# Performance work log

Measured on AMD Instinct MI355X. Metric: run time of the kernel, lower is better.

Reference implementation:

```python
import jax, jax.numpy as jnp
import numpy as np

D = 512
FV = 50000
EV = 50000
SRC = 128
TGT = 129  # BOS + 128 targets


def setup_inputs() -> dict:
    key = jax.random.key(0)
    ks = jax.random.split(key, 16)
    s = 0.02  # init scale
    return {
        "fnums": jax.random.randint(ks[0], (SRC,), 0, FV, dtype=jnp.int32),
        "enums": jax.random.randint(ks[1], (TGT,), 0, EV, dtype=jnp.int32),
        "emb_f": jax.random.normal(ks[2], (FV, D), jnp.float32) * s,
        "Wih_e": jax.random.normal(ks[3], (D, D), jnp.float32) * s,
        "Whh_e": jax.random.normal(ks[4], (D, D), jnp.float32) * s,
        "b_e": jnp.zeros((D,), jnp.float32),
        "h0_e": jax.random.normal(ks[5], (D,), jnp.float32) * s,
        "emb_d": jax.random.normal(ks[6], (EV, D), jnp.float32) * s,
        "Wih_d": jax.random.normal(ks[7], (D, D), jnp.float32) * s,
        "Whh_d": jax.random.normal(ks[8], (D, D), jnp.float32) * s,
        "b_d": jnp.zeros((D,), jnp.float32),
        "h0_d": jax.random.normal(ks[9], (D,), jnp.float32) * s,
        "Wm": jax.random.normal(ks[10], (D, 2 * D), jnp.float32) * s,
        "bm": jnp.zeros((D,), jnp.float32),
        "Wo": jax.random.normal(ks[11], (EV, D), jnp.float32) * s,
        "bo": jnp.zeros((EV,), jnp.float32),
    }


def reference(fnums, enums, emb_f, Wih_e, Whh_e, b_e, h0_e,
              emb_d, Wih_d, Whh_d, b_d, h0_d, Wm, bm, Wo, bo):
    # --- Encoder: vanilla tanh RNN over source embeddings ---
    xs = emb_f[fnums]  # (SRC, D)

    def enc_step(h, x):
        h2 = jnp.tanh(x @ Wih_e.T + h @ Whh_e.T + b_e)
        return h2, h2

    _, fencs = jax.lax.scan(enc_step, h0_e, xs)  # (SRC, D)

    # --- Decoder: teacher-forced log-probability of enums[1:] given enums[:-1] ---
    inp = enums[:-1]
    tgt = enums[1:]

    def dec_step(h, it):
        i, t = it
        e = emb_d[i]                                   # (D,)
        h2 = jnp.tanh(e @ Wih_d.T + h @ Whh_d.T + b_d)  # new RNN state o == h2
        scores = fencs @ h2                             # (SRC,) dot-product attention
        alpha = jax.nn.softmax(scores)
        c = alpha @ fencs                               # (D,) context
        m = jnp.tanh(jnp.concatenate([c, h2]) @ Wm.T + bm)
        lp = jax.nn.log_softmax(m @ Wo.T + bo)          # (EV,)
        return h2, lp[t]

    _, lps = jax.lax.scan(dec_step, h0_d, (inp, tgt))
    return jnp.sum(lps)  # scalar log-probability of the sentence pair
```

## Files before the change

### kernel.cpp

```cpp
#include <hip/hip_runtime.h>
#include <stdint.h>

#define D      512
#define NSTEP  128
#define EVOC   50000
#define VTILE  128
#define NBV    ((EVOC + VTILE - 1) / VTILE)
#define LDA_W  36
#define LDB_W  132
#define WM16   (D / 16)
#define WO16   ((EVOC + 15) / 16)

typedef unsigned int u32x4 __attribute__((ext_vector_type(4)));

__device__ inline int sdot4(int a, int b, int c) {
#if __has_builtin(__builtin_amdgcn_sdot4)
    return __builtin_amdgcn_sdot4(a, b, c, false);
#else
    int r = c;
    r += (int)(int8_t)(a)       * (int)(int8_t)(b);
    r += (int)(int8_t)(a >> 8)  * (int)(int8_t)(b >> 8);
    r += (int)(int8_t)(a >> 16) * (int)(int8_t)(b >> 16);
    r += (int)(int8_t)(a >> 24) * (int)(int8_t)(b >> 24);
    return r;
#endif
}

__device__ inline int sdot8(uint32_t a, uint32_t b, int c) {
#if __has_builtin(__builtin_amdgcn_sdot8)
    return __builtin_amdgcn_sdot8((int)a, (int)b, c, false);
#else
    int r = c;
    #pragma unroll
    for (int k = 0; k < 8; k++) {
        int av = ((int)(a << (28 - 4 * k))) >> 28;
        int bv = ((int)(b << (28 - 4 * k))) >> 28;
        r += av * bv;
    }
    return r;
#endif
}

__device__ inline int rdlane(uint32_t v, int k) {
#if __has_builtin(__builtin_amdgcn_readlane)
    return (int)__builtin_amdgcn_readlane(v, k);
#else
    return (int)__shfl((int)v, k, 64);
#endif
}

__device__ inline uint32_t pack4(float a, float b, float c, float d, float inv) {
    return  ((uint32_t)(uint8_t)(int8_t)__float2int_rn(a * inv)) |
            ((uint32_t)(uint8_t)(int8_t)__float2int_rn(b * inv) << 8) |
            ((uint32_t)(uint8_t)(int8_t)__float2int_rn(c * inv) << 16) |
            ((uint32_t)(uint8_t)(int8_t)__float2int_rn(d * inv) << 24);
}

__device__ inline float amax4(float4 v) {
    return fmaxf(fmaxf(fabsf(v.x), fabsf(v.y)), fmaxf(fabsf(v.z), fabsf(v.w)));
}

__global__ __launch_bounds__(256) void k_prep2(
        const float* __restrict__ We,   const float* __restrict__ Wd,
        const int* __restrict__ fnums,  const int* __restrict__ enums,
        const float* __restrict__ emb_f,const float* __restrict__ emb_d,
        const float* __restrict__ Wih_e,const float* __restrict__ Wih_d,
        const float* __restrict__ b_e,  const float* __restrict__ b_d,
        uint32_t* __restrict__ q4, float* __restrict__ qsc,
        float* __restrict__ pre_e, float* __restrict__ pre_d) {
    __shared__ float xl[D];
    int bid = blockIdx.x, t = threadIdx.x;
    if (bid < 256) {
        int rg = bid * 4 + (t >> 6);
        int which = rg >> 9, row = rg & 511;
        int lane = t & 63;
        const float* W = which ? Wd : We;
        const float* src = W + (size_t)row * D + lane * 8;
        float w[8];
        #pragma unroll
        for (int k = 0; k < 8; k++) w[k] = src[k];
        float m = 0.f;
        #pragma unroll
        for (int k = 0; k < 8; k++) m = fmaxf(m, fabsf(w[k]));
        for (int off = 32; off; off >>= 1) m = fmaxf(m, __shfl_xor(m, off));
        float inv = (m > 0.f) ? 7.f / m : 0.f;
        uint32_t word = 0;
        #pragma unroll
        for (int k = 0; k < 8; k++) {
            int q = max(-7, min(7, __float2int_rn(w[k] * inv)));
            word |= ((uint32_t)(q & 0xF)) << (4 * k);
        }
        int hf = lane >> 5, c = (lane & 31) >> 2, wi = lane & 3;
        q4[((size_t)which * 8192 + (size_t)c * 1024 + (hf << 9) + row) * 4 + wi] = word;
        if (lane == 0) qsc[which * D + row] = m / 7.f;
    } else {
        int bb = bid - 256;
        int kind = bb >> 7, s = bb & 127;
        const float* emb = kind ? emb_d : emb_f;
        int idx          = kind ? enums[s] : fnums[s];
        const float* W   = kind ? Wih_d : Wih_e;
        const float* b   = kind ? b_d : b_e;
        float* pre       = kind ? pre_d : pre_e;
        xl[t]       = emb[(size_t)idx * D + t];
        xl[t + 256] = emb[(size_t)idx * D + t + 256];
        __syncthreads();
        for (int rep = 0; rep < 2; rep++) {
            int o = t + rep * 256;
            float acc = b[o];
            const float4* Wr = (const float4*)(W + (size_t)o * D);
            #pragma unroll 8
            for (int k4 = 0; k4 < D / 4; k4++) {
                float4 w = Wr[k4];
                acc += w.x * xl[4*k4] + w.y * xl[4*k4+1] + w.z * xl[4*k4+2] + w.w * xl[4*k4+3];
            }
            pre[(size_t)s * D + o] = acc;
        }
    }
}

__global__ __launch_bounds__(1024)
__attribute__((amdgpu_waves_per_eu(4, 4)))
void k_scan_fused(
        const uint32_t* __restrict__ q4, const float* __restrict__ qsc,
        const float* __restrict__ pre_e, const float* __restrict__ pre_d,
        const float* __restrict__ h0_e, const float* __restrict__ h0_d,
        float* __restrict__ fencs, float* __restrict__ h2s,
        const float* __restrict__ Wm, const float* __restrict__ Wo,
        int8_t* __restrict__ wmq, float* __restrict__ wmsc,
        uint32_t* __restrict__ woq2, float* __restrict__ wosc) {
    __shared__ __align__(16) uint32_t wlds[16384];
    __shared__ __align__(4) uint32_t hq4[2][64];
    __shared__ int pacc[D];
    int bid = blockIdx.x, t = threadIdx.x;

    if (bid >= 2) {
        int lane = t & 63, sub = t >> 6;
        if (bid < 2 + WM16) {
            int row = (bid - 2) * 16 + sub;
            const float4* src = (const float4*)(Wm + (size_t)row * 2 * D);
            float4 a = src[lane], b = src[lane + 64], c = src[lane + 128], d2 = src[lane + 192];
            float m = fmaxf(fmaxf(amax4(a), amax4(b)), fmaxf(amax4(c), amax4(d2)));
            for (int off = 32; off; off >>= 1) m = fmaxf(m, __shfl_xor(m, off));
            float inv = (m > 0.f) ? 127.f / m : 0.f;
            uint32_t* dst = (uint32_t*)(wmq + (size_t)row * 2 * D);
            dst[lane]       = pack4(a.x, a.y, a.z, a.w, inv);
            dst[lane + 64]  = pack4(b.x, b.y, b.z, b.w, inv);
            dst[lane + 128] = pack4(c.x, c.y, c.z, c.w, inv);
            dst[lane + 192] = pack4(d2.x, d2.y, d2.z, d2.w, inv);
            if (lane == 0) wmsc[row] = m / 127.f;
        } else {
            int row = (bid - 2 - WM16) * 16 + sub;
            if (row < EVOC) {
                const float4* src = (const float4*)(Wo + (size_t)row * D);
                float4 v0 = src[lane], v1 = src[lane + 64];
                float m = fmaxf(amax4(v0), amax4(v1));
                for (int off = 32; off; off >>= 1) m = fmaxf(m, __shfl_xor(m, off));
                float inv = (m > 0.f) ? 127.f / m : 0.f;
                uint32_t w1 = pack4(v0.x, v0.y, v0.z, v0.w, inv);
                uint32_t w2 = pack4(v1.x, v1.y, v1.z, v1.w, inv);
                int wA = lane, wB = lane + 64;
                woq2[((size_t)(row >> 7) * 4 + (wA >> 5)) * 4096 + (size_t)(row & 127) * 32 + (wA & 31)] = w1;
                woq2[((size_t)(row >> 7) * 4 + (wB >> 5)) * 4096 + (size_t)(row & 127) * 32 + (wB & 31)] = w2;
                if (lane == 0) wosc[row] = m / 127.f;
            }
        }
        return;
    }

    int lane = t & 63;
    int hf = t >> 9;
    int r  = t & 511;
    int which = bid;
    const float* pre = which ? pre_d : pre_e;
    const float* h0  = which ? h0_d : h0_e;
    float*       hs  = which ? h2s : fencs;
    float sw = qsc[which * D + r] * (1.f / 7.f);
    const u32x4* wq = (const u32x4*)q4 + (size_t)which * 8192 + t;

    u32x4* wl = (u32x4*)wlds;
    #pragma unroll
    for (int c = 0; c < 4; c++) wl[c * 1024 + t] = wq[c * 1024];

    if (hf == 0) {
        float h0v = fminf(fmaxf(h0[r], -0.999f), 0.999f);
        int nib = max(-7, min(7, __float2int_rn(h0v * 7.f)));
        uint32_t mynib = (uint32_t)(nib & 0xF);
        uint32_t other = (uint32_t)__shfl_xor((int)mynib, 1);
        if (!(r & 1))
            ((uint8_t*)&hq4[0][0])[r >> 1] = (uint8_t)(mynib | (other << 4));
    }
    __syncthreads();

    int p = 0;
    for (int step = 0; step < NSTEP; step++) {
        uint32_t own = hq4[p][(hf << 5) | (lane & 31)];
        u32x4 g0 = wq[4 * 1024], g1 = wq[5 * 1024], g2 = wq[6 * 1024], g3 = wq[7 * 1024];
        u32x4 l0 = wl[t], l1 = wl[1024 + t], l2 = wl[2048 + t], l3 = wl[3072 + t];
        int a0 = 0, a1 = 0;
        #define DOTC(c, wv) {                                          \
            a0 = sdot8((wv).x, (uint32_t)rdlane(own, (c) * 4 + 0), a0);\
            a1 = sdot8((wv).y, (uint32_t)rdlane(own, (c) * 4 + 1), a1);\
            a0 = sdot8((wv).z, (uint32_t)rdlane(own, (c) * 4 + 2), a0);\
            a1 = sdot8((wv).w, (uint32_t)rdlane(own, (c) * 4 + 3), a1); }
        DOTC(0, l0) DOTC(1, l1) DOTC(2, l2) DOTC(3, l3)
        DOTC(4, g0) DOTC(5, g1) DOTC(6, g2) DOTC(7, g3)
        #undef DOTC
        int acc = a0 + a1;
        if (hf) pacc[r] = acc;
        __syncthreads();
        if (!hf) {
            int tot = acc + pacc[r];
            float h2 = tanhf(pre[(size_t)step * D + r] + (float)tot * sw);
            hs[(size_t)step * D + r] = h2;
            int nib = max(-7, min(7, __float2int_rn(h2 * 7.f)));
            uint32_t mynib = (uint32_t)(nib & 0xF);
            uint32_t other = (uint32_t)__shfl_xor((int)mynib, 1);
            if (!(r & 1))
                ((uint8_t*)&hq4[p ^ 1][0])[r >> 1] = (uint8_t)(mynib | (other << 4));
        }
        __syncthreads();
        p ^= 1;
    }
}

__global__ __launch_bounds__(512) void k_att1(
        const float* __restrict__ fencs, const float* __restrict__ h2s,
        int8_t* __restrict__ chq) {
    __shared__ float h2l[D], sc[NSTEP], red[64];
    __shared__ float ftile[32 * D];
    int s = blockIdx.x, t = threadIdx.x;
    h2l[t] = h2s[(size_t)s * D + t];
    __syncthreads();

    {
        int j = t >> 2, q = t & 3;
        const float4* fr = (const float4*)(fencs + (size_t)j * D + q * 128);
        const float4* hr = (const float4*)(h2l + q * 128);
        float acc = 0.f;
        #pragma unroll 8
        for (int k4 = 0; k4 < 32; k4++) {
            float4 f = fr[k4], hh = hr[k4];
            acc += f.x*hh.x + f.y*hh.y + f.z*hh.z + f.w*hh.w;
        }
        acc += __shfl_xor(acc, 1);
        acc += __shfl_xor(acc, 2);
        if (q == 0) sc[j] = acc;
    }
    __syncthreads();
    if (t < 64) {
        float m = fmaxf(sc[t], sc[t + 64]);
        for (int off = 32; off; off >>= 1) m = fmaxf(m, __shfl_xor(m, off));
        if (t == 0) red[0] = m;
    }
    __syncthreads();
    float mx = red[0];
    __syncthreads();
    if (t < NSTEP) sc[t] = expf(sc[t] - mx);
    __syncthreads();
    if (t < 64) {
        float v = sc[t] + sc[t + 64];
        for (int off = 32; off; off >>= 1) v += __shfl_xor(v, off);
        if (t == 0) red[0] = v;
    }
    __syncthreads();
    float inv = 1.0f / red[0];

    float cacc = 0.f;
    for (int jt = 0; jt < 4; jt++) {
        #pragma unroll
        for (int k = 0; k < 32; k++)
            ftile[t + k * D] = fencs[(size_t)jt * 32 * D + t + k * D];
        __syncthreads();
        #pragma unroll 8
        for (int j = 0; j < 32; j++)
            cacc += sc[jt * 32 + j] * ftile[j * D + t];
        __syncthreads();
    }
    float cv = cacc * inv;
    chq[(size_t)s * 2 * D + t]     = (int8_t)__float2int_rn(cv * 127.f);
    chq[(size_t)s * 2 * D + D + t] = (int8_t)__float2int_rn(h2l[t] * 127.f);
}

__global__ __launch_bounds__(512) void k_att2(
        const int8_t* __restrict__ chq, const int8_t* __restrict__ wmq,
        const float* __restrict__ wmsc, const float* __restrict__ bm,
        int8_t* __restrict__ mq) {
    __shared__ __align__(16) uint32_t a_s[128 * LDA_W];
    __shared__ __align__(16) uint32_t b_s[32 * LDB_W];
    int t = threadIdx.x;
    int v0 = blockIdx.x * VTILE;
    int ti = t >> 5, tj = t & 31;
    int lrow = t >> 3, lq = t & 7;
    int acc[8][4] = {};

    for (int kc = 0; kc < 8; kc++) {
        #pragma unroll
        for (int rep = 0; rep < 2; rep++) {
            int row = lrow + rep * 64;
            uint4 av = *(const uint4*)(chq + (size_t)row * 2 * D + kc * 128 + lq * 16);
            *(uint4*)&a_s[row * LDA_W + lq * 4] = av;
            int v = v0 + row;
            uint4 bv = *(const uint4*)(wmq + (size_t)v * 2 * D + kc * 128 + lq * 16);
            b_s[(lq*4+0) * LDB_W + row] = bv.x;
            b_s[(lq*4+1) * LDB_W + row] = bv.y;
            b_s[(lq*4+2) * LDB_W + row] = bv.z;
            b_s[(lq*4+3) * LDB_W + row] = bv.w;
        }
        __syncthreads();
        #pragma unroll
        for (int q = 0; q < 8; q++) {
            uint4 aw[8];
            #pragma unroll
            for (int i = 0; i < 8; i++)
                aw[i] = *(const uint4*)&a_s[(ti*8 + i) * LDA_W + q*4];
            #pragma unroll
            for (int k4 = 0; k4 < 4; k4++) {
                uint4 bw = *(const uint4*)&b_s[(q*4 + k4) * LDB_W + tj * 4];
                #pragma unroll
                for (int i = 0; i < 8; i++) {
                    uint32_t a = (k4 == 0) ? aw[i].x : (k4 == 1) ? aw[i].y
                               : (k4 == 2) ? aw[i].z : aw[i].w;
                    acc[i][0] = sdot4((int)a, (int)bw.x, acc[i][0]);
                    acc[i][1] = sdot4((int)a, (int)bw.y, acc[i][1]);
                    acc[i][2] = sdot4((int)a, (int)bw.z, acc[i][2]);
                    acc[i][3] = sdot4((int)a, (int)bw.w, acc[i][3]);
                }
            }
        }
        __syncthreads();
    }

    float sw4[4], bm4[4];
    #pragma unroll
    for (int jj = 0; jj < 4; jj++) {
        int col = v0 + tj * 4 + jj;
        sw4[jj] = wmsc[col] * (1.f / (127.f * 127.f));
        bm4[jj] = bm[col];
    }
    #pragma unroll
    for (int i = 0; i < 8; i++) {
        int s = ti * 8 + i;
        float m0 = tanhf((float)acc[i][0] * sw4[0] + bm4[0]);
        float m1 = tanhf((float)acc[i][1] * sw4[1] + bm4[1]);
        float m2 = tanhf((float)acc[i][2] * sw4[2] + bm4[2]);
        float m3 = tanhf((float)acc[i][3] * sw4[3] + bm4[3]);
        ((uint32_t*)mq)[(size_t)s * (D / 4) + (v0 >> 2) + tj] = pack4(m0, m1, m2, m3, 127.f);
    }
}

__global__ __launch_bounds__(512) void k_logits(
        const int8_t* __restrict__ mq, const uint32_t* __restrict__ woq2,
        const float* __restrict__ wosc, const float* __restrict__ bo,
        const int* __restrict__ enums,
        float* __restrict__ pmax, float* __restrict__ psum, float* __restrict__ pick) {
    __shared__ __align__(16) uint32_t a_s[128 * LDA_W];
    __shared__ __align__(16) uint32_t b_s[32 * LDB_W];
    int b = blockIdx.x, t = threadIdx.x;
    int v0 = b * VTILE;
    int ti = t >> 5, tj = t & 31;
    int lrow = t >> 3, lq = t & 7;
    int acc[8][4] = {};

    for (int kc = 0; kc < 4; kc++) {
        const uint4* bsrc = (const uint4*)(woq2 + ((size_t)b * 4 + kc) * 4096);
        #pragma unroll
        for (int rep = 0; rep < 2; rep++) {
            int row = lrow + rep * 64;
            uint4 av = *(const uint4*)(mq + (size_t)row * D + kc * 128 + lq * 16);
            *(uint4*)&a_s[row * LDA_W + lq * 4] = av;
            uint4 bv = bsrc[t + rep * 512];
            b_s[(lq*4+0) * LDB_W + row] = bv.x;
            b_s[(lq*4+1) * LDB_W + row] = bv.y;
            b_s[(lq*4+2) * LDB_W + row] = bv.z;
            b_s[(lq*4+3) * LDB_W + row] = bv.w;
        }
        __syncthreads();
        #pragma unroll
        for (int q = 0; q < 8; q++) {
            uint4 aw[8];
            #pragma unroll
            for (int i = 0; i < 8; i++)
                aw[i] = *(const uint4*)&a_s[(ti*8 + i) * LDA_W + q*4];
            #pragma unroll
            for (int k4 = 0; k4 < 4; k4++) {
                uint4 bw = *(const uint4*)&b_s[(q*4 + k4) * LDB_W + tj * 4];
                #pragma unroll
                for (int i = 0; i < 8; i++) {
                    uint32_t a = (k4 == 0) ? aw[i].x : (k4 == 1) ? aw[i].y
                               : (k4 == 2) ? aw[i].z : aw[i].w;
                    acc[i][0] = sdot4((int)a, (int)bw.x, acc[i][0]);
                    acc[i][1] = sdot4((int)a, (int)bw.y, acc[i][1]);
                    acc[i][2] = sdot4((int)a, (int)bw.z, acc[i][2]);
                    acc[i][3] = sdot4((int)a, (int)bw.w, acc[i][3]);
                }
            }
        }
        __syncthreads();
    }

    float sw4[4], bo4[4];
    int vld[4];
    #pragma unroll
    for (int jj = 0; jj < 4; jj++) {
        int v = v0 + tj * 4 + jj;
        vld[jj] = (v < EVOC);
        sw4[jj] = vld[jj] ? wosc[v] * (1.f / 127.f) : 0.f;
        bo4[jj] = vld[jj] ? bo[v] : 0.f;
    }
    #pragma unroll
    for (int i = 0; i < 8; i++) {
        int s = ti * 8 + i;
        float l[4];
        float mx = -1e30f;
        #pragma unroll
        for (int jj = 0; jj < 4; jj++) {
            l[jj] = vld[jj] ? (float)acc[i][jj] * sw4[jj] + bo4[jj] : -1e30f;
            mx = fmaxf(mx, l[jj]);
        }
        #pragma unroll
        for (int off = 1; off < 32; off <<= 1) mx = fmaxf(mx, __shfl_xor(mx, off));
        float sm = 0.f;
        #pragma unroll
        for (int jj = 0; jj < 4; jj++)
            if (vld[jj]) sm += expf(l[jj] - mx);
        #pragma unroll
        for (int off = 1; off < 32; off <<= 1) sm += __shfl_xor(sm, off);
        if (tj == 0) { pmax[b * NSTEP + s] = mx; psum[b * NSTEP + s] = sm; }
        int tgt = enums[s + 1];
        if (tgt >= v0 && tgt < v0 + VTILE) {
            int c = tgt - v0;
            if ((c >> 2) == tj) pick[s] = l[c & 3];
        }
    }
}

__global__ __launch_bounds__(256) void k_final_par(
        const float* __restrict__ pmax, const float* __restrict__ psum,
        const float* __restrict__ pick, float* __restrict__ lp) {
    __shared__ float red[8];
    int s = blockIdx.x, t = threadIdx.x;
    float M = -1e30f;
    for (int b = t; b < NBV; b += 256) M = fmaxf(M, pmax[b * NSTEP + s]);
    for (int off = 32; off; off >>= 1) M = fmaxf(M, __shfl_xor(M, off));
    if ((t & 63) == 0) red[t >> 6] = M;
    __syncthreads();
    M = fmaxf(fmaxf(red[0], red[1]), fmaxf(red[2], red[3]));
    float S = 0.f;
    for (int b = t; b < NBV; b += 256) S += psum[b * NSTEP + s] * expf(pmax[b * NSTEP + s] - M);
    for (int off = 32; off; off >>= 1) S += __shfl_xor(S, off);
    if ((t & 63) == 0) red[4 + (t >> 6)] = S;
    __syncthreads();
    if (t == 0) {
        S = red[4] + red[5] + red[6] + red[7];
        lp[s] = pick[s] - (M + logf(S));
    }
}

__global__ void k_final_sum(const float* __restrict__ lp, float* __restrict__ out) {
    __shared__ float red[NSTEP];
    int t = threadIdx.x;
    red[t] = lp[t];
    __syncthreads();
    for (int off = 64; off > 0; off >>= 1) {
        if (t < off) red[t] += red[t + off];
        __syncthreads();
    }
    if (t == 0) out[0] = red[0];
}

extern "C" void kernel_launch(void* const* d_in, const int* in_sizes, int n_in,
                              void* d_out, int out_size, void* d_ws, size_t ws_size,
                              hipStream_t stream) {
    const int*   fnums = (const int*)  d_in[0];
    const int*   enums = (const int*)  d_in[1];
    const float* emb_f = (const float*)d_in[2];
    const float* Wih_e = (const float*)d_in[3];
    const float* Whh_e = (const float*)d_in[4];
    const float* b_e   = (const float*)d_in[5];
    const float* h0_e  = (const float*)d_in[6];
    const float* emb_d = (const float*)d_in[7];
    const float* Wih_d = (const float*)d_in[8];
    const float* Whh_d = (const float*)d_in[9];
    const float* b_d   = (const float*)d_in[10];
    const float* h0_d  = (const float*)d_in[11];
    const float* Wm    = (const float*)d_in[12];
    const float* bm    = (const float*)d_in[13];
    const float* Wo    = (const float*)d_in[14];
    const float* bo    = (const float*)d_in[15];

    float* ws = (float*)d_ws;
    float* pre_e = ws;
    float* pre_d = ws + 65536;
    float* fencs = ws + 131072;
    float* h2s   = ws + 196608;
    float* pmax  = ws + 262144;
    float* psum  = ws + 312192;
    float* pick  = ws + 362240;
    float* lp    = ws + 362368;
    float* qsc   = ws + 362496;
    float* wmsc  = ws + 363520;
    float* wosc  = ws + 364032;
    uint32_t* q4 = (uint32_t*)(ws + 414080);
    int8_t*   wmq  = (int8_t*)(ws + 479616);
    int8_t*   chq  = (int8_t*)(ws + 610688);
    int8_t*   mq   = (int8_t*)(ws + 643456);
    uint32_t* woq2 = (uint32_t*)(ws + 659840);

    k_prep2<<<dim3(512), dim3(256), 0, stream>>>(
        Whh_e, Whh_d, fnums, enums, emb_f, emb_d, Wih_e, Wih_d, b_e, b_d,
        q4, qsc, pre_e, pre_d);
    k_scan_fused<<<dim3(2 + WM16 + WO16), dim3(1024), 0, stream>>>(
        q4, qsc, pre_e, pre_d, h0_e, h0_d, fencs, h2s,
        Wm, Wo, wmq, wmsc, woq2, wosc);
    k_att1<<<dim3(NSTEP), dim3(512), 0, stream>>>(fencs, h2s, chq);
    k_att2<<<dim3(4), dim3(512), 0, stream>>>(chq, wmq, wmsc, bm, mq);
    k_logits<<<dim3(NBV), dim3(512), 0, stream>>>(mq, woq2, wosc, bo, enums, pmax, psum, pick);
    k_final_par<<<dim3(NSTEP), dim3(256), 0, stream>>>(pmax, psum, pick, lp);
    k_final_sum<<<dim3(1), dim3(NSTEP), 0, stream>>>(lp, (float*)d_out);
}
```

Measured before the change: 273.4 us.

## Use one thread per hidden row in the recurrent scan to drop the cross-half reduction

The recurrent scan kernel drops from 1024 to 512 threads per block, so each thread computes a full 512-wide row dot product instead of half of one. This removes the shared-memory partial-sum exchange and one block barrier per step. Half of the quantized weight row stays in LDS and half is loaded from global memory each step. The int4 weight layout produced by the prep kernel is changed to match, and the side blocks that quantize Wm and Wo now handle 8 rows each, so twice as many blocks are launched. The cost is twice the serial dot-product work per thread and more registers per thread.

```diff
diff --git a/kernel.cpp b/kernel.cpp
--- a/kernel.cpp
+++ b/kernel.cpp
@@ -8,8 +8,8 @@
 #define NBV    ((EVOC + VTILE - 1) / VTILE)
 #define LDA_W  36
 #define LDB_W  132
-#define WM16   (D / 16)
-#define WO16   ((EVOC + 15) / 16)
+#define WM8    (D / 8)
+#define WO8    ((EVOC + 7) / 8)
 
 typedef unsigned int u32x4 __attribute__((ext_vector_type(4)));
 
@@ -90,8 +90,7 @@
             int q = max(-7, min(7, __float2int_rn(w[k] * inv)));
             word |= ((uint32_t)(q & 0xF)) << (4 * k);
         }
-        int hf = lane >> 5, c = (lane & 31) >> 2, wi = lane & 3;
-        q4[((size_t)which * 8192 + (size_t)c * 1024 + (hf << 9) + row) * 4 + wi] = word;
+        q4[((size_t)which * 8192 + (size_t)(lane >> 2) * 512 + row) * 4 + (lane & 3)] = word;
         if (lane == 0) qsc[which * D + row] = m / 7.f;
     } else {
         int bb = bid - 256;
@@ -118,7 +117,7 @@
     }
 }
 
-__global__ __launch_bounds__(1024)
+__global__ __launch_bounds__(512)
 __attribute__((amdgpu_waves_per_eu(4, 4)))
 void k_scan_fused(
         const uint32_t* __restrict__ q4, const float* __restrict__ qsc,
@@ -130,13 +129,12 @@
         uint32_t* __restrict__ woq2, float* __restrict__ wosc) {
     __shared__ __align__(16) uint32_t wlds[16384];
     __shared__ __align__(4) uint32_t hq4[2][64];
-    __shared__ int pacc[D];
     int bid = blockIdx.x, t = threadIdx.x;
 
     if (bid >= 2) {
         int lane = t & 63, sub = t >> 6;
-        if (bid < 2 + WM16) {
-            int row = (bid - 2) * 16 + sub;
+        if (bid < 2 + WM8) {
+            int row = (bid - 2) * 8 + sub;
             const float4* src = (const float4*)(Wm + (size_t)row * 2 * D);
             float4 a = src[lane], b = src[lane + 64], c = src[lane + 128], d2 = src[lane + 192];
             float m = fmaxf(fmaxf(amax4(a), amax4(b)), fmaxf(amax4(c), amax4(d2)));
@@ -149,7 +147,7 @@
             dst[lane + 192] = pack4(d2.x, d2.y, d2.z, d2.w, inv);
             if (lane == 0) wmsc[row] = m / 127.f;
         } else {
-            int row = (bid - 2 - WM16) * 16 + sub;
+            int row = (bid - 2 - WM8) * 8 + sub;
             if (row < EVOC) {
                 const float4* src = (const float4*)(Wo + (size_t)row * D);
                 float4 v0 = src[lane], v1 = src[lane + 64];
@@ -168,8 +166,7 @@
     }
 
     int lane = t & 63;
-    int hf = t >> 9;
-    int r  = t & 511;
+    int r = t;
     int which = bid;
     const float* pre = which ? pre_d : pre_e;
     const float* h0  = which ? h0_d : h0_e;
@@ -179,9 +176,9 @@
 
     u32x4* wl = (u32x4*)wlds;
     #pragma unroll
-    for (int c = 0; c < 4; c++) wl[c * 1024 + t] = wq[c * 1024];
-
-    if (hf == 0) {
+    for (int c = 0; c < 8; c++) wl[c * 512 + t] = wq[c * 512];
+
+    {
         float h0v = fminf(fmaxf(h0[r], -0.999f), 0.999f);
         int nib = max(-7, min(7, __float2int_rn(h0v * 7.f)));
         uint32_t mynib = (uint32_t)(nib & 0xF);
@@ -193,31 +190,34 @@
 
     int p = 0;
     for (int step = 0; step < NSTEP; step++) {
-        uint32_t own = hq4[p][(hf << 5) | (lane & 31)];
-        u32x4 g0 = wq[4 * 1024], g1 = wq[5 * 1024], g2 = wq[6 * 1024], g3 = wq[7 * 1024];
-        u32x4 l0 = wl[t], l1 = wl[1024 + t], l2 = wl[2048 + t], l3 = wl[3072 + t];
-        int a0 = 0, a1 = 0;
-        #define DOTC(c, wv) {                                          \
-            a0 = sdot8((wv).x, (uint32_t)rdlane(own, (c) * 4 + 0), a0);\
-            a1 = sdot8((wv).y, (uint32_t)rdlane(own, (c) * 4 + 1), a1);\
-            a0 = sdot8((wv).z, (uint32_t)rdlane(own, (c) * 4 + 2), a0);\
-            a1 = sdot8((wv).w, (uint32_t)rdlane(own, (c) * 4 + 3), a1); }
-        DOTC(0, l0) DOTC(1, l1) DOTC(2, l2) DOTC(3, l3)
-        DOTC(4, g0) DOTC(5, g1) DOTC(6, g2) DOTC(7, g3)
+        uint32_t own = hq4[p][lane];
+        u32x4 g0 = wq[8 * 512],  g1 = wq[9 * 512],  g2 = wq[10 * 512], g3 = wq[11 * 512];
+        u32x4 g4 = wq[12 * 512], g5 = wq[13 * 512], g6 = wq[14 * 512], g7 = wq[15 * 512];
+        int a0 = 0, a1 = 0, a2 = 0, a3 = 0;
+        #define DOTC(c, wv) {                                           \
+            a0 = sdot8((wv).x, (uint32_t)rdlane(own, (c) * 4 + 0), a0); \
+            a1 = sdot8((wv).y, (uint32_t)rdlane(own, (c) * 4 + 1), a1); \
+            a2 = sdot8((wv).z, (uint32_t)rdlane(own, (c) * 4 + 2), a2); \
+            a3 = sdot8((wv).w, (uint32_t)rdlane(own, (c) * 4 + 3), a3); }
+        {
+            u32x4 l0 = wl[t],            l1 = wl[512 + t];
+            u32x4 l2 = wl[2 * 512 + t],  l3 = wl[3 * 512 + t];
+            u32x4 l4 = wl[4 * 512 + t],  l5 = wl[5 * 512 + t];
+            u32x4 l6 = wl[6 * 512 + t],  l7 = wl[7 * 512 + t];
+            DOTC(0, l0) DOTC(1, l1) DOTC(2, l2) DOTC(3, l3)
+            DOTC(4, l4) DOTC(5, l5) DOTC(6, l6) DOTC(7, l7)
+        }
+        DOTC(8, g0)  DOTC(9, g1)  DOTC(10, g2) DOTC(11, g3)
+        DOTC(12, g4) DOTC(13, g5) DOTC(14, g6) DOTC(15, g7)
         #undef DOTC
-        int acc = a0 + a1;
-        if (hf) pacc[r] = acc;
-        __syncthreads();
-        if (!hf) {
-            int tot = acc + pacc[r];
-            float h2 = tanhf(pre[(size_t)step * D + r] + (float)tot * sw);
-            hs[(size_t)step * D + r] = h2;
-            int nib = max(-7, min(7, __float2int_rn(h2 * 7.f)));
-            uint32_t mynib = (uint32_t)(nib & 0xF);
-            uint32_t other = (uint32_t)__shfl_xor((int)mynib, 1);
-            if (!(r & 1))
-                ((uint8_t*)&hq4[p ^ 1][0])[r >> 1] = (uint8_t)(mynib | (other << 4));
-        }
+        int acc = (a0 + a1) + (a2 + a3);
+        float h2 = tanhf(pre[(size_t)step * D + r] + (float)acc * sw);
+        hs[(size_t)step * D + r] = h2;
+        int nib = max(-7, min(7, __float2int_rn(h2 * 7.f)));
+        uint32_t mynib = (uint32_t)(nib & 0xF);
+        uint32_t other = (uint32_t)__shfl_xor((int)mynib, 1);
+        if (!(r & 1))
+            ((uint8_t*)&hq4[p ^ 1][0])[r >> 1] = (uint8_t)(mynib | (other << 4));
         __syncthreads();
         p ^= 1;
     }
@@ -509,7 +509,7 @@
     k_prep2<<<dim3(512), dim3(256), 0, stream>>>(
         Whh_e, Whh_d, fnums, enums, emb_f, emb_d, Wih_e, Wih_d, b_e, b_d,
         q4, qsc, pre_e, pre_d);
-    k_scan_fused<<<dim3(2 + WM16 + WO16), dim3(1024), 0, stream>>>(
+    k_scan_fused<<<dim3(2 + WM8 + WO8), dim3(512), 0, stream>>>(
         q4, qsc, pre_e, pre_d, h0_e, h0_d, fencs, h2s,
         Wm, Wo, wmq, wmsc, woq2, wosc);
     k_att1<<<dim3(NSTEP), dim3(512), 0, stream>>>(fencs, h2s, chq);
```

Result: faster. 242.7 us (-11.2%).
